# Performance work log

Measured on AMD Instinct MI355X. Metric: run time of the kernel, lower is better.

The kernel has to match this reference:

```python
import jax, jax.numpy as jnp
import numpy as np

B, T, P = 4096, 128, 2
D_m = D_g = D_p = D_e = 256


def gru_cell(x, h, w_ih, w_hh, b_ih, b_hh):
    # PyTorch GRUCell math
    gi = x @ w_ih.T + b_ih          # [N, 3H]
    gh = h @ w_hh.T + b_hh          # [N, 3H]
    ir, iz, inn = jnp.split(gi, 3, axis=1)
    hr, hz, hn = jnp.split(gh, 3, axis=1)
    r = jax.nn.sigmoid(ir + hr)
    z = jax.nn.sigmoid(iz + hz)
    n = jnp.tanh(inn + r * hn)
    return (1.0 - z) * n + z * h


def _gru_params(key, in_dim, hid):
    k1, k2, k3, k4 = jax.random.split(key, 4)
    s = 1.0 / np.sqrt(hid)
    u = lambda k, shp: jax.random.uniform(k, shp, jnp.float32, -s, s)
    return u(k1, (3 * hid, in_dim)), u(k2, (3 * hid, hid)), u(k3, (3 * hid,)), u(k4, (3 * hid,))


def setup_inputs() -> dict:
    key = jax.random.key(0)
    ks = jax.random.split(key, 10)
    U = jax.random.normal(ks[0], (B, D_m), jnp.float32)
    qm_idx = jax.random.randint(ks[1], (B,), 0, P)
    g_hist = jax.random.normal(ks[2], (T, B, D_g), jnp.float32)
    q0 = jax.random.normal(ks[3], (B, P, D_p), jnp.float32)
    e0 = jax.random.normal(ks[4], (B, D_e), jnp.float32)
    wg = _gru_params(ks[5], D_m + D_p, D_g)
    wp = _gru_params(ks[6], D_m + D_g, D_p)
    we = _gru_params(ks[7], D_p, D_e)
    sa = 1.0 / np.sqrt(D_g)
    attn_w = jax.random.uniform(ks[8], (1, D_g), jnp.float32, -sa, sa)
    return {
        "U": U, "qm_idx": qm_idx, "g_hist": g_hist, "q0": q0, "e0": e0,
        "wg_ih": wg[0], "wg_hh": wg[1], "bg_ih": wg[2], "bg_hh": wg[3],
        "wp_ih": wp[0], "wp_hh": wp[1], "bp_ih": wp[2], "bp_hh": wp[3],
        "we_ih": we[0], "we_hh": we[1], "be_ih": we[2], "be_hh": we[3],
        "attn_w": attn_w,
    }


def reference(U, qm_idx, g_hist, q0, e0,
              wg_ih, wg_hh, bg_ih, bg_hh,
              wp_ih, wp_hh, bp_ih, bp_hh,
              we_ih, we_hh, be_ih, be_hh,
              attn_w):
    b_idx = jnp.arange(U.shape[0])
    qmask = jax.nn.one_hot(qm_idx, P, dtype=U.dtype)             # [B, P]
    # _select_parties: gather the speaking party's state
    q0_sel = q0[b_idx, qm_idx]                                    # [B, D_p]
    # global GRU step (g_hist non-empty -> hidden = g_hist[-1])
    g_ = gru_cell(jnp.concatenate([U, q0_sel], axis=1), g_hist[-1],
                  wg_ih, wg_hh, bg_ih, bg_hh)                     # [B, D_g]
    # SimpleAttention over history: softmax over time of a scalar score
    scale = jnp.einsum('tbd,od->tb', g_hist, attn_w)              # [T, B]
    alpha_t = jax.nn.softmax(scale, axis=0)                       # [T, B]
    c_ = jnp.einsum('tb,tbd->bd', alpha_t, g_hist)                # [B, D_g]
    alpha = alpha_t.T[:, None, :]                                 # [B, 1, T]
    # party GRU applied to every party slot
    U_c = jnp.concatenate([U, c_], axis=1)                        # [B, D_m+D_g]
    U_c_exp = jnp.broadcast_to(U_c[:, None, :], (U.shape[0], P, U_c.shape[1]))
    qs_ = gru_cell(U_c_exp.reshape(-1, D_m + D_g), q0.reshape(-1, D_p),
                   wp_ih, wp_hh, bp_ih, bp_hh).reshape(U.shape[0], P, D_p)
    # listener_state=False: listeners keep q0; speaker slot takes qs_
    qm = qmask[..., None]
    q_ = q0 * (1.0 - qm) + qs_ * qm                               # [B, P, D_p]
    # emotion GRU on the speaking party's updated state
    e_ = gru_cell(q_[b_idx, qm_idx], e0, we_ih, we_hh, be_ih, be_hh)  # [B, D_e]
    return g_, q_, e_, alpha
```

## Files before the change

kernel.cpp:

```cpp
#include <hip/hip_runtime.h>
#include <hip/hip_bf16.h>
#include <cstdint>
#include <cstddef>

#define B_N   4096
#define T_N   128
#define P_N   2
#define D     256
#define NG    768
#define BD    (B_N * D)

typedef __attribute__((ext_vector_type(4))) float f32x4;
typedef __attribute__((ext_vector_type(8))) short bf16x8;
typedef __attribute__((ext_vector_type(8))) unsigned short ushort8;

__device__ __forceinline__ unsigned short f2bf(float f) {
    __hip_bfloat16 h = __float2bfloat16(f);
    return *reinterpret_cast<unsigned short*>(&h);
}

struct CvtJobs {
    const float*     src[9];
    unsigned short*  dst[9];
    int              n[9];
};

__global__ __launch_bounds__(256) void cvt_batch(CvtJobs jobs)
{
    const int j = blockIdx.y;
    const int i = (blockIdx.x * 256 + threadIdx.x) * 8;
    if (i >= jobs.n[j]) return;
    const float4* s = reinterpret_cast<const float4*>(jobs.src[j] + i);
    const float4 v0 = s[0], v1 = s[1];
    ushort8 o = { f2bf(v0.x), f2bf(v0.y), f2bf(v0.z), f2bf(v0.w),
                  f2bf(v1.x), f2bf(v1.y), f2bf(v1.z), f2bf(v1.w) };
    *reinterpret_cast<ushort8*>(jobs.dst[j] + i) = o;
}

__global__ __launch_bounds__(256) void attn_kernel(
    const float* __restrict__ g_hist, const float* __restrict__ attn_w,
    unsigned short* __restrict__ c_bf, float* __restrict__ alpha_out)
{
    const int lane = threadIdx.x & 63;
    const int wid  = threadIdx.x >> 6;
    const int b    = blockIdx.x * 4 + wid;

    const float4 w4 = *reinterpret_cast<const float4*>(attn_w + lane * 4);
    const float* gbase = g_hist + (size_t)b * D + lane * 4;

    float  m = -INFINITY, l = 0.f;
    float4 acc = {0.f, 0.f, 0.f, 0.f};
    float  s0 = 0.f, s1 = 0.f;

    auto step = [&](int t, const float4& g) {
        float dot = g.x * w4.x + g.y * w4.y + g.z * w4.z + g.w * w4.w;
        #pragma unroll
        for (int off = 32; off >= 1; off >>= 1)
            dot += __shfl_xor(dot, off, 64);
        const float mn   = fmaxf(m, dot);
        const float corr = __expf(m - mn);
        const float p    = __expf(dot - mn);
        l = l * corr + p;
        acc.x = fmaf(p, g.x, acc.x * corr);
        acc.y = fmaf(p, g.y, acc.y * corr);
        acc.z = fmaf(p, g.z, acc.z * corr);
        acc.w = fmaf(p, g.w, acc.w * corr);
        m = mn;
        if ((t & 63) == lane) { if (t & 64) s1 = dot; else s0 = dot; }
    };

    for (int t = 0; t < T_N; t += 2) {
        const float4 g0 = *reinterpret_cast<const float4*>(gbase + (size_t)t * BD);
        const float4 g1 = *reinterpret_cast<const float4*>(gbase + (size_t)(t + 1) * BD);
        step(t, g0);
        step(t + 1, g1);
    }

    const float rl = 1.f / l;
    ushort4 cv = { f2bf(acc.x * rl), f2bf(acc.y * rl),
                   f2bf(acc.z * rl), f2bf(acc.w * rl) };
    *reinterpret_cast<ushort4*>(c_bf + (size_t)b * D + lane * 4) = cv;
    alpha_out[(size_t)b * T_N + lane]      = __expf(s0 - m) * rl;
    alpha_out[(size_t)b * T_N + 64 + lane] = __expf(s1 - m) * rl;
}

__global__ __launch_bounds__(256) void gru_gemm_mfma(
    const unsigned short* __restrict__ A0, const unsigned short* __restrict__ A1,
    const unsigned short* __restrict__ Wi, int ldwi, int Ki,
    const float* __restrict__ bi,
    const unsigned short* __restrict__ Ah, const unsigned short* __restrict__ Wh,
    const float* __restrict__ bh,
    float* __restrict__ gi, float* __restrict__ gh)
{
    const int phase = blockIdx.z;
    const unsigned short* W = phase ? Wh : Wi;
    const int ldw  = phase ? D : ldwi;
    const int K    = phase ? D : Ki;
    const float* bias = phase ? bh : bi;
    float* Cout    = phase ? gh : gi;

    const int r0 = blockIdx.x * 128;
    const int n0 = blockIdx.y * 128;

    __shared__ unsigned short As[128 * 32];
    __shared__ unsigned short Bs[128 * 32];

    const int tid  = threadIdx.x;
    const int lane = tid & 63;
    const int wid  = tid >> 6;
    const int wr   = wid >> 1, wc = wid & 1;

    const int st_row_in_call = lane >> 2;
    const int st_p           = lane & 3;

    f32x4 acc[4][4] = {};

    for (int kt = 0; kt < K; kt += 32) {
        const unsigned short* Asrc;
        if (phase) {
            Asrc = Ah + (size_t)r0 * D + kt;
        } else {
            const unsigned short* Ap = (kt < D) ? A0 : A1;
            Asrc = Ap + (size_t)r0 * D + (kt & (D - 1));
        }
        const unsigned short* Wsrc = W + (size_t)n0 * ldw + kt;

        #pragma unroll
        for (int c = 0; c < 2; ++c) {
            const int row = wid * 32 + c * 16 + st_row_in_call;
            const int scol = (st_p ^ ((row >> 1) & 3)) * 8;
            __builtin_amdgcn_global_load_lds(
                (const __attribute__((address_space(1))) void*)
                    (Asrc + (size_t)row * D + scol),
                (__attribute__((address_space(3))) void*)
                    (As + wid * 1024 + c * 512), 16, 0, 0);
            __builtin_amdgcn_global_load_lds(
                (const __attribute__((address_space(1))) void*)
                    (Wsrc + (size_t)row * ldw + scol),
                (__attribute__((address_space(3))) void*)
                    (Bs + wid * 1024 + c * 512), 16, 0, 0);
        }
        __syncthreads();

        const int s  = lane >> 4;
        const int fr = lane & 15;
        bf16x8 a[4], b[4];
        #pragma unroll
        for (int m = 0; m < 4; ++m) {
            const int row = wr * 64 + m * 16 + fr;
            const int ph  = s ^ ((row >> 1) & 3);
            a[m] = *reinterpret_cast<const bf16x8*>(&As[row * 32 + ph * 8]);
        }
        #pragma unroll
        for (int n = 0; n < 4; ++n) {
            const int row = wc * 64 + n * 16 + fr;
            const int ph  = s ^ ((row >> 1) & 3);
            b[n] = *reinterpret_cast<const bf16x8*>(&Bs[row * 32 + ph * 8]);
        }
        #pragma unroll
        for (int m = 0; m < 4; ++m)
            #pragma unroll
            for (int n = 0; n < 4; ++n)
                acc[m][n] = __builtin_amdgcn_mfma_f32_16x16x32_bf16(
                    a[m], b[n], acc[m][n], 0, 0, 0);
        __syncthreads();
    }

    const int cr = (lane >> 4) * 4;
    const int cc = lane & 15;
    #pragma unroll
    for (int m = 0; m < 4; ++m) {
        #pragma unroll
        for (int n = 0; n < 4; ++n) {
            const int col = n0 + wc * 64 + n * 16 + cc;
            const float bv = bias[col];
            #pragma unroll
            for (int q = 0; q < 4; ++q) {
                const int row = r0 + wr * 64 + m * 16 + cr + q;
                Cout[(size_t)row * NG + col] = acc[m][n][q] + bv;
            }
        }
    }
}

__global__ __launch_bounds__(256) void gru_gate(
    const float* __restrict__ gi, const float* __restrict__ gh,
    const float* __restrict__ h,
    float* __restrict__ out_f32, unsigned short* __restrict__ out_bf,
    float* __restrict__ scatter_base, const int* __restrict__ scatter_idx)
{
    const int i   = blockIdx.x * 256 + threadIdx.x;
    const int row = i >> 8;
    const int j   = i & 255;
    const size_t g0 = (size_t)row * NG + j;

    const float ir = gi[g0], iz = gi[g0 + 256], in_ = gi[g0 + 512];
    const float hr = gh[g0], hz = gh[g0 + 256], hn  = gh[g0 + 512];
    const float hv = h[(size_t)row * D + j];

    const float r = 1.f / (1.f + __expf(-(ir + hr)));
    const float z = 1.f / (1.f + __expf(-(iz + hz)));
    const float n = tanhf(in_ + r * hn);
    const float val = (1.f - z) * n + z * hv;

    if (out_f32) out_f32[(size_t)row * D + j] = val;
    if (out_bf)  out_bf[(size_t)row * D + j]  = f2bf(val);
    if (scatter_idx)
        scatter_base[((size_t)row * P_N + scatter_idx[row]) * D + j] = val;
}

__global__ __launch_bounds__(256) void gather_q0(
    const float* __restrict__ q0, const int* __restrict__ qm,
    float* __restrict__ q0_sel, unsigned short* __restrict__ q0_sel_bf)
{
    const int i   = blockIdx.x * 256 + threadIdx.x;
    const int row = i >> 6;
    const int j   = (i & 63) * 4;
    const float4 v = *reinterpret_cast<const float4*>(
        q0 + ((size_t)row * P_N + qm[row]) * D + j);
    *reinterpret_cast<float4*>(q0_sel + (size_t)row * D + j) = v;
    ushort4 bv = { f2bf(v.x), f2bf(v.y), f2bf(v.z), f2bf(v.w) };
    *reinterpret_cast<ushort4*>(q0_sel_bf + (size_t)row * D + j) = bv;
}

__global__ __launch_bounds__(256) void copy4(
    const float* __restrict__ src, float* __restrict__ dst, int n4)
{
    const int i = blockIdx.x * 256 + threadIdx.x;
    if (i < n4)
        reinterpret_cast<float4*>(dst)[i] =
            reinterpret_cast<const float4*>(src)[i];
}

extern "C" void kernel_launch(void* const* d_in, const int* in_sizes, int n_in,
                              void* d_out, int out_size, void* d_ws, size_t ws_size,
                              hipStream_t stream)
{
    const float* U      = (const float*)d_in[0];
    const int*   qm     = (const int*)  d_in[1];
    const float* g_hist = (const float*)d_in[2];
    const float* q0     = (const float*)d_in[3];
    const float* e0     = (const float*)d_in[4];
    const float* wg_ih  = (const float*)d_in[5];
    const float* wg_hh  = (const float*)d_in[6];
    const float* bg_ih  = (const float*)d_in[7];
    const float* bg_hh  = (const float*)d_in[8];
    const float* wp_ih  = (const float*)d_in[9];
    const float* wp_hh  = (const float*)d_in[10];
    const float* bp_ih  = (const float*)d_in[11];
    const float* bp_hh  = (const float*)d_in[12];
    const float* we_ih  = (const float*)d_in[13];
    const float* we_hh  = (const float*)d_in[14];
    const float* be_ih  = (const float*)d_in[15];
    const float* be_hh  = (const float*)d_in[16];
    const float* attn_w = (const float*)d_in[17];

    float* out   = (float*)d_out;
    float* g_out = out;
    float* q_out = out + 1048576;
    float* e_out = out + 3145728;
    float* a_out = out + 4194304;

    float* ws     = (float*)d_ws;
    float* gibuf  = ws;
    float* ghbuf  = ws + 3145728;
    float* q0self = ws + 6291456;
    unsigned short* bf = (unsigned short*)(ws + 7340032);
    unsigned short* U_bf     = bf;
    unsigned short* e0_bf    = bf + 1048576;
    unsigned short* glast_bf = bf + 2097152;
    unsigned short* q0sel_bf = bf + 3145728;
    unsigned short* c_bf     = bf + 4194304;
    unsigned short* qssel_bf = bf + 5242880;
    unsigned short* wgih_bf  = bf + 6291456;
    unsigned short* wpih_bf  = bf + 6684672;
    unsigned short* wghh_bf  = bf + 7077888;
    unsigned short* wphh_bf  = bf + 7274496;
    unsigned short* weih_bf  = bf + 7471104;
    unsigned short* wehh_bf  = bf + 7667712;

    const float* g_last = g_hist + (size_t)(T_N - 1) * BD;

    const dim3 blk(256);
    const dim3 gridGemm(B_N / 128, NG / 128, 2);

    CvtJobs jobs;
    jobs.src[0] = wg_ih;  jobs.dst[0] = wgih_bf;  jobs.n[0] = NG * 512;
    jobs.src[1] = wg_hh;  jobs.dst[1] = wghh_bf;  jobs.n[1] = NG * 256;
    jobs.src[2] = wp_ih;  jobs.dst[2] = wpih_bf;  jobs.n[2] = NG * 512;
    jobs.src[3] = wp_hh;  jobs.dst[3] = wphh_bf;  jobs.n[3] = NG * 256;
    jobs.src[4] = we_ih;  jobs.dst[4] = weih_bf;  jobs.n[4] = NG * 256;
    jobs.src[5] = we_hh;  jobs.dst[5] = wehh_bf;  jobs.n[5] = NG * 256;
    jobs.src[6] = U;      jobs.dst[6] = U_bf;     jobs.n[6] = B_N * D;
    jobs.src[7] = e0;     jobs.dst[7] = e0_bf;    jobs.n[7] = B_N * D;
    jobs.src[8] = g_last; jobs.dst[8] = glast_bf; jobs.n[8] = B_N * D;
    cvt_batch<<<dim3(B_N * D / 8 / 256, 9), blk, 0, stream>>>(jobs);

    gather_q0<<<B_N * D / 4 / 256, blk, 0, stream>>>(q0, qm, q0self, q0sel_bf);
    copy4<<<(B_N * P_N * D / 4 + 255) / 256, blk, 0, stream>>>(
        q0, q_out, B_N * P_N * D / 4);
    attn_kernel<<<B_N / 4, blk, 0, stream>>>(g_hist, attn_w, c_bf, a_out);

    gru_gemm_mfma<<<gridGemm, blk, 0, stream>>>(
        U_bf, q0sel_bf, wgih_bf, 512, 512, bg_ih,
        glast_bf, wghh_bf, bg_hh, gibuf, ghbuf);
    gru_gate<<<B_N, blk, 0, stream>>>(
        gibuf, ghbuf, g_last, g_out, nullptr, nullptr, nullptr);

    gru_gemm_mfma<<<gridGemm, blk, 0, stream>>>(
        U_bf, c_bf, wpih_bf, 512, 512, bp_ih,
        q0sel_bf, wphh_bf, bp_hh, gibuf, ghbuf);
    gru_gate<<<B_N, blk, 0, stream>>>(
        gibuf, ghbuf, q0self, nullptr, qssel_bf, q_out, qm);

    gru_gemm_mfma<<<gridGemm, blk, 0, stream>>>(
        qssel_bf, nullptr, weih_bf, 256, 256, be_ih,
        e0_bf, wehh_bf, be_hh, gibuf, ghbuf);
    gru_gate<<<B_N, blk, 0, stream>>>(
        gibuf, ghbuf, e0, e_out, nullptr, nullptr, nullptr);
}
```

Measured before the change: 196.5 us.

## Fuse GRU gate math into MFMA GEMM epilogue with gate-interleaved column tiles

The separate GEMM and gate kernels are merged into one templated kernel. Each block computes a 32-column slice of all three gates for both the input and hidden GEMMs, and applies the GRU nonlinearity in registers. This removes the fp32 gi/gh intermediate buffers (about 24 MB of writes plus reads per GRU), the q0 copy kernel, and three launches. The party-GRU epilogue writes both party slots directly. The cost is a smaller per-block N tile, 12 accumulator tiles per wave (more registers), and narrower 32-column output stores.

```diff
diff --git a/kernel.cpp b/kernel.cpp
--- a/kernel.cpp
+++ b/kernel.cpp
@@ -84,152 +84,139 @@
     alpha_out[(size_t)b * T_N + 64 + lane] = __expf(s1 - m) * rl;
 }
 
-__global__ __launch_bounds__(256) void gru_gemm_mfma(
-    const unsigned short* __restrict__ A0, const unsigned short* __restrict__ A1,
+template<int MODE>
+__global__ __launch_bounds__(256) void fused_gru(
+    const unsigned short* __restrict__ A0,
+    const unsigned short* __restrict__ A1,
     const unsigned short* __restrict__ Wi, int ldwi, int Ki,
     const float* __restrict__ bi,
-    const unsigned short* __restrict__ Ah, const unsigned short* __restrict__ Wh,
+    const unsigned short* __restrict__ Ah,
+    const unsigned short* __restrict__ Wh,
     const float* __restrict__ bh,
-    float* __restrict__ gi, float* __restrict__ gh)
-{
-    const int phase = blockIdx.z;
-    const unsigned short* W = phase ? Wh : Wi;
-    const int ldw  = phase ? D : ldwi;
-    const int K    = phase ? D : Ki;
-    const float* bias = phase ? bh : bi;
-    float* Cout    = phase ? gh : gi;
-
+    const float* __restrict__ hsrc,
+    const int*  __restrict__ qm,
+    float* __restrict__ out_f32,
+    unsigned short* __restrict__ out_bf)
+{
     const int r0 = blockIdx.x * 128;
-    const int n0 = blockIdx.y * 128;
+    const int c0 = blockIdx.y * 32;
 
     __shared__ unsigned short As[128 * 32];
-    __shared__ unsigned short Bs[128 * 32];
+    __shared__ unsigned short Ws[128 * 32];
 
     const int tid  = threadIdx.x;
     const int lane = tid & 63;
     const int wid  = tid >> 6;
-    const int wr   = wid >> 1, wc = wid & 1;
-
-    const int st_row_in_call = lane >> 2;
-    const int st_p           = lane & 3;
-
-    f32x4 acc[4][4] = {};
-
-    for (int kt = 0; kt < K; kt += 32) {
-        const unsigned short* Asrc;
-        if (phase) {
-            Asrc = Ah + (size_t)r0 * D + kt;
-        } else {
-            const unsigned short* Ap = (kt < D) ? A0 : A1;
-            Asrc = Ap + (size_t)r0 * D + (kt & (D - 1));
-        }
-        const unsigned short* Wsrc = W + (size_t)n0 * ldw + kt;
-
+
+    const int st_row = lane >> 2;
+    const int st_p   = lane & 3;
+
+    f32x4 accI[2][6] = {};
+    f32x4 accH[2][6] = {};
+
+    auto kstep = [&](const unsigned short* Apart, int kcolA, int kcolW,
+                     const unsigned short* W, int ldw, f32x4 (&acc)[2][6]) {
         #pragma unroll
         for (int c = 0; c < 2; ++c) {
-            const int row = wid * 32 + c * 16 + st_row_in_call;
+            const int row  = wid * 32 + c * 16 + st_row;
             const int scol = (st_p ^ ((row >> 1) & 3)) * 8;
             __builtin_amdgcn_global_load_lds(
                 (const __attribute__((address_space(1))) void*)
-                    (Asrc + (size_t)row * D + scol),
+                    (Apart + (size_t)(r0 + row) * D + kcolA + scol),
                 (__attribute__((address_space(3))) void*)
                     (As + wid * 1024 + c * 512), 16, 0, 0);
+            int grp = row >> 5; if (grp == 3) grp = 2;
+            const int wrow = grp * 256 + c0 + (row & 31);
             __builtin_amdgcn_global_load_lds(
                 (const __attribute__((address_space(1))) void*)
-                    (Wsrc + (size_t)row * ldw + scol),
+                    (W + (size_t)wrow * ldw + kcolW + scol),
                 (__attribute__((address_space(3))) void*)
-                    (Bs + wid * 1024 + c * 512), 16, 0, 0);
+                    (Ws + wid * 1024 + c * 512), 16, 0, 0);
         }
         __syncthreads();
 
         const int s  = lane >> 4;
         const int fr = lane & 15;
-        bf16x8 a[4], b[4];
-        #pragma unroll
-        for (int m = 0; m < 4; ++m) {
-            const int row = wr * 64 + m * 16 + fr;
+        bf16x8 a[2], b[6];
+        #pragma unroll
+        for (int m = 0; m < 2; ++m) {
+            const int row = wid * 32 + m * 16 + fr;
             const int ph  = s ^ ((row >> 1) & 3);
             a[m] = *reinterpret_cast<const bf16x8*>(&As[row * 32 + ph * 8]);
         }
         #pragma unroll
-        for (int n = 0; n < 4; ++n) {
-            const int row = wc * 64 + n * 16 + fr;
+        for (int j = 0; j < 6; ++j) {
+            const int row = j * 16 + fr;
             const int ph  = s ^ ((row >> 1) & 3);
-            b[n] = *reinterpret_cast<const bf16x8*>(&Bs[row * 32 + ph * 8]);
-        }
-        #pragma unroll
-        for (int m = 0; m < 4; ++m)
+            b[j] = *reinterpret_cast<const bf16x8*>(&Ws[row * 32 + ph * 8]);
+        }
+        #pragma unroll
+        for (int m = 0; m < 2; ++m)
             #pragma unroll
-            for (int n = 0; n < 4; ++n)
-                acc[m][n] = __builtin_amdgcn_mfma_f32_16x16x32_bf16(
-                    a[m], b[n], acc[m][n], 0, 0, 0);
+            for (int j = 0; j < 6; ++j)
+                acc[m][j] = __builtin_amdgcn_mfma_f32_16x16x32_bf16(
+                    a[m], b[j], acc[m][j], 0, 0, 0);
         __syncthreads();
+    };
+
+    for (int kt = 0; kt < Ki; kt += 32) {
+        const unsigned short* Ap = (kt < D) ? A0 : A1;
+        kstep(Ap, kt & (D - 1), kt, Wi, ldwi, accI);
     }
+    for (int kt = 0; kt < D; kt += 32)
+        kstep(Ah, kt, kt, Wh, D, accH);
 
     const int cr = (lane >> 4) * 4;
     const int cc = lane & 15;
     #pragma unroll
-    for (int m = 0; m < 4; ++m) {
-        #pragma unroll
-        for (int n = 0; n < 4; ++n) {
-            const int col = n0 + wc * 64 + n * 16 + cc;
-            const float bv = bias[col];
+    for (int m = 0; m < 2; ++m) {
+        #pragma unroll
+        for (int jj = 0; jj < 2; ++jj) {
+            const int col = c0 + jj * 16 + cc;
+            const float bir = bi[col],       bhr = bh[col];
+            const float biz = bi[col + 256], bhz = bh[col + 256];
+            const float bin = bi[col + 512], bhn = bh[col + 512];
             #pragma unroll
             for (int q = 0; q < 4; ++q) {
-                const int row = r0 + wr * 64 + m * 16 + cr + q;
-                Cout[(size_t)row * NG + col] = acc[m][n][q] + bv;
+                const int row = r0 + wid * 32 + m * 16 + cr + q;
+                const float ir  = accI[m][jj][q]     + bir;
+                const float hr  = accH[m][jj][q]     + bhr;
+                const float iz  = accI[m][jj + 2][q] + biz;
+                const float hz  = accH[m][jj + 2][q] + bhz;
+                const float in_ = accI[m][jj + 4][q] + bin;
+                const float hn  = accH[m][jj + 4][q] + bhn;
+                const float rg = 1.f / (1.f + __expf(-(ir + hr)));
+                const float zg = 1.f / (1.f + __expf(-(iz + hz)));
+                const float ng = tanhf(in_ + rg * hn);
+                if (MODE == 1) {
+                    const int p = qm[row];
+                    const float hv  = hsrc[(size_t)row * 512 + (size_t)p * 256 + col];
+                    const float ov  = hsrc[(size_t)row * 512 + (size_t)(1 - p) * 256 + col];
+                    const float val = (1.f - zg) * ng + zg * hv;
+                    out_f32[(size_t)row * 512 + (size_t)p * 256 + col]       = val;
+                    out_f32[(size_t)row * 512 + (size_t)(1 - p) * 256 + col] = ov;
+                    out_bf[(size_t)row * 256 + col] = f2bf(val);
+                } else {
+                    const float hv  = hsrc[(size_t)row * 256 + col];
+                    const float val = (1.f - zg) * ng + zg * hv;
+                    out_f32[(size_t)row * 256 + col] = val;
+                }
             }
         }
     }
-}
-
-__global__ __launch_bounds__(256) void gru_gate(
-    const float* __restrict__ gi, const float* __restrict__ gh,
-    const float* __restrict__ h,
-    float* __restrict__ out_f32, unsigned short* __restrict__ out_bf,
-    float* __restrict__ scatter_base, const int* __restrict__ scatter_idx)
-{
-    const int i   = blockIdx.x * 256 + threadIdx.x;
-    const int row = i >> 8;
-    const int j   = i & 255;
-    const size_t g0 = (size_t)row * NG + j;
-
-    const float ir = gi[g0], iz = gi[g0 + 256], in_ = gi[g0 + 512];
-    const float hr = gh[g0], hz = gh[g0 + 256], hn  = gh[g0 + 512];
-    const float hv = h[(size_t)row * D + j];
-
-    const float r = 1.f / (1.f + __expf(-(ir + hr)));
-    const float z = 1.f / (1.f + __expf(-(iz + hz)));
-    const float n = tanhf(in_ + r * hn);
-    const float val = (1.f - z) * n + z * hv;
-
-    if (out_f32) out_f32[(size_t)row * D + j] = val;
-    if (out_bf)  out_bf[(size_t)row * D + j]  = f2bf(val);
-    if (scatter_idx)
-        scatter_base[((size_t)row * P_N + scatter_idx[row]) * D + j] = val;
 }
 
 __global__ __launch_bounds__(256) void gather_q0(
     const float* __restrict__ q0, const int* __restrict__ qm,
-    float* __restrict__ q0_sel, unsigned short* __restrict__ q0_sel_bf)
+    unsigned short* __restrict__ q0_sel_bf)
 {
     const int i   = blockIdx.x * 256 + threadIdx.x;
     const int row = i >> 6;
     const int j   = (i & 63) * 4;
     const float4 v = *reinterpret_cast<const float4*>(
         q0 + ((size_t)row * P_N + qm[row]) * D + j);
-    *reinterpret_cast<float4*>(q0_sel + (size_t)row * D + j) = v;
     ushort4 bv = { f2bf(v.x), f2bf(v.y), f2bf(v.z), f2bf(v.w) };
     *reinterpret_cast<ushort4*>(q0_sel_bf + (size_t)row * D + j) = bv;
-}
-
-__global__ __launch_bounds__(256) void copy4(
-    const float* __restrict__ src, float* __restrict__ dst, int n4)
-{
-    const int i = blockIdx.x * 256 + threadIdx.x;
-    if (i < n4)
-        reinterpret_cast<float4*>(dst)[i] =
-            reinterpret_cast<const float4*>(src)[i];
 }
 
 extern "C" void kernel_launch(void* const* d_in, const int* in_sizes, int n_in,
@@ -261,11 +248,7 @@
     float* e_out = out + 3145728;
     float* a_out = out + 4194304;
 
-    float* ws     = (float*)d_ws;
-    float* gibuf  = ws;
-    float* ghbuf  = ws + 3145728;
-    float* q0self = ws + 6291456;
-    unsigned short* bf = (unsigned short*)(ws + 7340032);
+    unsigned short* bf = (unsigned short*)d_ws;
     unsigned short* U_bf     = bf;
     unsigned short* e0_bf    = bf + 1048576;
     unsigned short* glast_bf = bf + 2097152;
@@ -282,7 +265,7 @@
     const float* g_last = g_hist + (size_t)(T_N - 1) * BD;
 
     const dim3 blk(256);
-    const dim3 gridGemm(B_N / 128, NG / 128, 2);
+    const dim3 gridGru(B_N / 128, D / 32);
 
     CvtJobs jobs;
     jobs.src[0] = wg_ih;  jobs.dst[0] = wgih_bf;  jobs.n[0] = NG * 512;
@@ -296,26 +279,21 @@
     jobs.src[8] = g_last; jobs.dst[8] = glast_bf; jobs.n[8] = B_N * D;
     cvt_batch<<<dim3(B_N * D / 8 / 256, 9), blk, 0, stream>>>(jobs);
 
-    gather_q0<<<B_N * D / 4 / 256, blk, 0, stream>>>(q0, qm, q0self, q0sel_bf);
-    copy4<<<(B_N * P_N * D / 4 + 255) / 256, blk, 0, stream>>>(
-        q0, q_out, B_N * P_N * D / 4);
+    gather_q0<<<B_N * D / 4 / 256, blk, 0, stream>>>(q0, qm, q0sel_bf);
     attn_kernel<<<B_N / 4, blk, 0, stream>>>(g_hist, attn_w, c_bf, a_out);
 
-    gru_gemm_mfma<<<gridGemm, blk, 0, stream>>>(
+    fused_gru<0><<<gridGru, blk, 0, stream>>>(
         U_bf, q0sel_bf, wgih_bf, 512, 512, bg_ih,
-        glast_bf, wghh_bf, bg_hh, gibuf, ghbuf);
-    gru_gate<<<B_N, blk, 0, stream>>>(
-        gibuf, ghbuf, g_last, g_out, nullptr, nullptr, nullptr);
-
-    gru_gemm_mfma<<<gridGemm, blk, 0, stream>>>(
+        glast_bf, wghh_bf, bg_hh,
+        g_last, nullptr, g_out, nullptr);
+
+    fused_gru<1><<<gridGru, blk, 0, stream>>>(
         U_bf, c_bf, wpih_bf, 512, 512, bp_ih,
-        q0sel_bf, wphh_bf, bp_hh, gibuf, ghbuf);
-    gru_gate<<<B_N, blk, 0, stream>>>(
-        gibuf, ghbuf, q0self, nullptr, qssel_bf, q_out, qm);
-
-    gru_gemm_mfma<<<gridGemm, blk, 0, stream>>>(
+        q0sel_bf, wphh_bf, bp_hh,
+        q0, qm, q_out, qssel_bf);
+
+    fused_gru<0><<<gridGru, blk, 0, stream>>>(
         qssel_bf, nullptr, weih_bf, 256, 256, be_ih,
-        e0_bf, wehh_bf, be_hh, gibuf, ghbuf);
-    gru_gate<<<B_N, blk, 0, stream>>>(
-        gibuf, ghbuf, e0, e_out, nullptr, nullptr, nullptr);
-}
+        e0_bf, wehh_bf, be_hh,
+        e0, nullptr, e_out, nullptr);
+}
```

Result: faster. 184.5 us (-6.1%).
